# Optimization experiments

Measured on AMD Instinct MI355X. Metric: run time of the kernel, lower is better.

Reference implementation:

```python
import jax, jax.numpy as jnp
import numpy as np


def setup_inputs() -> dict:
    key = jax.random.key(0)
    k1, k2, k3 = jax.random.split(key, 3)
    B, N, F, O = 2048, 50000, 256, 24
    x = jax.random.normal(k1, (B, F), dtype=jnp.float32)
    X_train = jax.random.normal(k2, (N, F), dtype=jnp.float32)
    Y_train = jax.random.normal(k3, (N, O), dtype=jnp.float32)
    return {"x": x, "X_train": X_train, "Y_train": Y_train}


def reference(x, X_train, Y_train):
    # x: [B, F] (already flat), X_train: [N, F], Y_train: [N, O]
    B = x.shape[0]
    x_flat = x.reshape(B, -1)
    # Squared Euclidean distances via expansion: ||a||^2 + ||b||^2 - 2 a.b
    # (monotone in true distance, so argmin is identical to cdist+argmin)
    x2 = jnp.sum(x_flat * x_flat, axis=1, keepdims=True)          # [B, 1]
    t2 = jnp.sum(X_train * X_train, axis=1)                        # [N]
    cross = x_flat @ X_train.T                                     # [B, N]
    d2 = x2 + t2[None, :] - 2.0 * cross                            # [B, N]
    nearest = jnp.argmin(d2, axis=1)                               # [B]
    y_pred = Y_train[nearest]                                      # [B, O]
    return y_pred
```

## Files before the change

kernel.cpp:

```cpp
#include <hip/hip_runtime.h>
#include <stdint.h>

typedef unsigned short u16;
typedef unsigned int   u32;
typedef unsigned long long u64;

#define F_DIM 256
#define O_DIM 24
#define MARGIN  3.0f
#define FMARGIN 3.0f
#define WCAP 512
#define NWAVE_CAP 4096

#define AS1 __attribute__((address_space(1)))
#define AS3 __attribute__((address_space(3)))

typedef __bf16 bf16x8 __attribute__((ext_vector_type(8)));
typedef float  f32x4  __attribute__((ext_vector_type(4)));

__device__ __forceinline__ u32 ordf(float s) {
    u32 b = __float_as_uint(s);
    return (b & 0x80000000u) ? ~b : (b | 0x80000000u);
}
__device__ __forceinline__ float iordf(u32 e) {
    return __uint_as_float((e & 0x80000000u) ? (e ^ 0x80000000u) : ~e);
}
__device__ __forceinline__ u16 f2bf(float f) {
    u32 u = __float_as_uint(f);
    u32 r = (u + 0x7FFFu + ((u >> 16) & 1u)) >> 16;
    return (u16)r;
}

__global__ void init_kernel(u64* best, u32* gminu, int B) {
    int i = blockIdx.x * blockDim.x + threadIdx.x;
    if (i < B) { best[i] = ~0ull; if (gminu) gminu[i] = ordf(1e30f); }
}

__global__ void t2_kernel(const float* __restrict__ X, float* __restrict__ t2,
                          int N, int Npad) {
    int tid = threadIdx.x;
    int row = blockIdx.x * 4 + (tid >> 6);
    int lane = tid & 63;
    if (row >= Npad) return;
    if (row >= N) { if (lane == 0) t2[row] = 1e30f; return; }
    float4 v = ((const float4*)(X + (size_t)row * F_DIM))[lane];
    float s = v.x * v.x + v.y * v.y + v.z * v.z + v.w * v.w;
    #pragma unroll
    for (int off = 32; off > 0; off >>= 1) s += __shfl_down(s, off, 64);
    if (lane == 0) t2[row] = s;
}

__global__ __launch_bounds__(256) void convert_tile(const float* __restrict__ src,
        u16* __restrict__ dst, float* __restrict__ t2out, int nrows, int do_t2,
        u64* best, u32* gminu, int ninit) {
    __shared__ u16 tl[8192];
    const int tid = threadIdx.x;
    const int t = blockIdx.x, p = blockIdx.y;
    if (best) {
        int id = (p * gridDim.x + t) * 256 + tid;
        if (id < ninit) { best[id] = ~0ull; gminu[id] = ordf(1e30f); }
    }
    const int w = tid >> 6, L = tid & 63;
    const int col = L * 4;
    const int ks = col >> 5, j = col & 7, lhi = ((col >> 3) & 3) << 4;
    #pragma unroll
    for (int i = 0; i < 8; ++i) {
        int rloc = i * 4 + w;
        int grow = t * 128 + p * 32 + rloc;
        float4 v = make_float4(0.f, 0.f, 0.f, 0.f);
        if (grow < nrows) v = *(const float4*)(src + (size_t)grow * F_DIM + col);
        if (do_t2) {
            float s = v.x * v.x + v.y * v.y + v.z * v.z + v.w * v.w;
            #pragma unroll
            for (int off = 32; off > 0; off >>= 1) s += __shfl_down(s, off, 64);
            if (L == 0) t2out[grow] = (grow < nrows) ? s : 1e30f;
        }
        u16* q = &tl[ks * 1024 + (rloc >> 4) * 512 + (((rloc & 15) | lhi)) * 8 + j];
        q[0] = f2bf(v.x); q[1] = f2bf(v.y); q[2] = f2bf(v.z); q[3] = f2bf(v.w);
    }
    __syncthreads();
    const uint4* s4 = (const uint4*)tl;
    uint4* d4 = (uint4*)(dst + (size_t)t * 32768);
    #pragma unroll
    for (int v = 0; v < 4; ++v) {
        int lin = v * 256 + tid;
        int ksc = lin >> 7, subl = (lin >> 6) & 1, lane = lin & 63;
        d4[(ksc * 8 + 2 * p + subl) * 64 + lane] = s4[lin];
    }
}

__global__ __launch_bounds__(512, 2) void knn_mfma(
    const u16* __restrict__ xbf, const u16* __restrict__ xtbf,
    const float* __restrict__ t2, u32* __restrict__ gminu,
    u32* __restrict__ wavecnt, u64* __restrict__ cands,
    int ntiles , int nch)
{
    __shared__ u16 sB[2][8192];

    const int tid = threadIdx.x;
    const int L = tid & 63, w = tid >> 6;
    const int lid = blockIdx.x;
    const int mbcnt = (int)(gridDim.x) / nch;
    int mb, chunk;
    if (nch == 64 && mbcnt == 8) {
        const int xg = lid & 7, slot = lid >> 3;
        chunk = xg * 8 + (slot >> 3);
        mb = slot & 7;
    } else {
        mb = lid % mbcnt;
        chunk = lid / mbcnt;
    }
    const int gwave = (mb * 64 + chunk) * 8 + w;
    const int t0 = (int)(((long long)chunk * ntiles) / nch);
    const int t1 = (int)(((long long)(chunk + 1) * ntiles) / nch);

    #define TBASE_U32(nt) ((const AS1 u32*)xtbf + (size_t)((nt) >> 2) * 16384 \
                           + (size_t)(((nt) >> 1) & 1) * 1024 + (size_t)((nt) & 1) * 512)

    #define STAGE(buf, nt) do {                                                        \
        const AS1 u32* gp_ = TBASE_U32(nt);                                            \
        AS3 u32* lb_ = (AS3 u32*)&sB[buf][0];                                          \
        _Pragma("unroll")                                                              \
        for (int j = 0; j < 2; ++j) {                                                  \
            const int unit = j * 8 + w;                                                \
            __builtin_amdgcn_global_load_lds(                                          \
                gp_ + (size_t)(unit >> 1) * 2048 + (size_t)(unit & 1) * 256            \
                    + (size_t)L * 4,                                                   \
                lb_ + unit * 256, 16, 0, 0);                                           \
        }                                                                              \
    } while (0)

    STAGE(0, t0);

    bf16x8 areg[16];
    {
        const int t128 = mb * 2 + (w >> 2);
        const u16* base = xbf + (size_t)t128 * 32768 + (size_t)(w & 3) * 1024 + (size_t)L * 8;
        #pragma unroll
        for (int ks = 0; ks < 8; ++ks)
            #pragma unroll
            for (int i = 0; i < 2; ++i)
                areg[ks * 2 + i] = *(const bf16x8*)(base + ks * 4096 + i * 512);
    }

    float rowmin_reg[2][4];
    #pragma unroll
    for (int i = 0; i < 2; ++i)
        #pragma unroll
        for (int r = 0; r < 4; ++r) rowmin_reg[i][r] = 1e30f;

    u32 wcount = 0;
    u64* const wreg = cands + (size_t)gwave * WCAP;

    __syncthreads();

    for (int nt = t0; nt < t1; ++nt) {
        const int cur = (nt - t0) & 1;
        if (nt + 1 < t1) STAGE(cur ^ 1, nt + 1);

        float t2v[2];
        #pragma unroll
        for (int c = 0; c < 2; ++c) t2v[c] = t2[nt * 32 + (L & 15) + c * 16];

        f32x4 acc[2][2];
        #pragma unroll
        for (int i = 0; i < 2; ++i)
            #pragma unroll
            for (int c = 0; c < 2; ++c)
                #pragma unroll
                for (int r = 0; r < 4; ++r) acc[i][c][r] = 0.f;

        #pragma unroll
        for (int ks = 0; ks < 8; ++ks) {
            bf16x8 bc[2];
            #pragma unroll
            for (int c = 0; c < 2; ++c)
                bc[c] = *(const bf16x8*)&sB[cur][ks * 1024 + c * 512 + L * 8];
            #pragma unroll
            for (int i = 0; i < 2; ++i)
                #pragma unroll
                for (int c = 0; c < 2; ++c)
                    acc[i][c] = __builtin_amdgcn_mfma_f32_16x16x32_bf16(areg[ks * 2 + i], bc[c], acc[i][c], 0, 0, 0);
        }

        const int colb = nt * 32 + (L & 15);
        float r4[2][4];
        #pragma unroll
        for (int i = 0; i < 2; ++i) {
            #pragma unroll
            for (int r = 0; r < 4; ++r) r4[i][r] = 1e30f;
            #pragma unroll
            for (int c = 0; c < 2; ++c)
                #pragma unroll
                for (int r = 0; r < 4; ++r)
                    r4[i][r] = fminf(r4[i][r], fmaf(-2.f, acc[i][c][r], t2v[c]));
        }

        float thb[2][4];
        if (nt == t0) {
            #pragma unroll
            for (int i = 0; i < 2; ++i)
                #pragma unroll
                for (int r = 0; r < 4; ++r) rowmin_reg[i][r] = r4[i][r];
            #pragma unroll
            for (int st = 1; st <= 8; st <<= 1)
                #pragma unroll
                for (int i = 0; i < 2; ++i)
                    #pragma unroll
                    for (int r = 0; r < 4; ++r)
                        rowmin_reg[i][r] = fminf(rowmin_reg[i][r], __shfl_xor(rowmin_reg[i][r], st, 64));
            #pragma unroll
            for (int i = 0; i < 2; ++i)
                #pragma unroll
                for (int r = 0; r < 4; ++r) thb[i][r] = rowmin_reg[i][r];
        } else {
            #pragma unroll
            for (int i = 0; i < 2; ++i)
                #pragma unroll
                for (int r = 0; r < 4; ++r) thb[i][r] = fminf(rowmin_reg[i][r], r4[i][r]);
        }

        bool anyhit = false;
        #pragma unroll
        for (int i = 0; i < 2; ++i)
            #pragma unroll
            for (int r = 0; r < 4; ++r)
                anyhit = anyhit || (r4[i][r] < thb[i][r] + MARGIN);

        if (__any(anyhit)) {
            u32 cnt = 0;
            #pragma unroll
            for (int i = 0; i < 2; ++i)
                #pragma unroll
                for (int r = 0; r < 4; ++r) {
                    float th = thb[i][r] + MARGIN;
                    if (r4[i][r] < th) {
                        #pragma unroll
                        for (int c = 0; c < 2; ++c)
                            cnt += (fmaf(-2.f, acc[i][c][r], t2v[c]) < th) ? 1u : 0u;
                    }
                }
            u32 pre = cnt;
            #pragma unroll
            for (int d = 1; d < 64; d <<= 1) {
                u32 v = __shfl_up(pre, d, 64);
                if (L >= d) pre += v;
            }
            u32 total = __shfl(pre, 63, 64);
            u32 woff = wcount + pre - cnt;
            #pragma unroll
            for (int i = 0; i < 2; ++i)
                #pragma unroll
                for (int r = 0; r < 4; ++r) {
                    float th = thb[i][r] + MARGIN;
                    if (r4[i][r] < th) {
                        const int q = mb * 256 + w * 32 + i * 16 + (L >> 4) * 4 + r;
                        #pragma unroll
                        for (int c = 0; c < 2; ++c) {
                            float s = fmaf(-2.f, acc[i][c][r], t2v[c]);
                            if (s < th) {
                                if (woff < WCAP)
                                    wreg[woff] = ((u64)__float_as_uint(s) << 32)
                                               | (u64)(((u32)q << 16) | (u32)(colb + c * 16));
                                woff++;
                            }
                        }
                    }
                }
            wcount += total;
        }

        #pragma unroll
        for (int i = 0; i < 2; ++i)
            #pragma unroll
            for (int r = 0; r < 4; ++r)
                rowmin_reg[i][r] = fminf(rowmin_reg[i][r], r4[i][r]);
        if (((nt - t0) & 3) == 3) {
            #pragma unroll
            for (int st = 1; st <= 8; st <<= 1)
                #pragma unroll
                for (int i = 0; i < 2; ++i)
                    #pragma unroll
                    for (int r = 0; r < 4; ++r)
                        rowmin_reg[i][r] = fminf(rowmin_reg[i][r], __shfl_xor(rowmin_reg[i][r], st, 64));
        }

        __syncthreads();
    }

    #pragma unroll
    for (int st = 1; st <= 8; st <<= 1)
        #pragma unroll
        for (int i = 0; i < 2; ++i)
            #pragma unroll
            for (int r = 0; r < 4; ++r)
                rowmin_reg[i][r] = fminf(rowmin_reg[i][r], __shfl_xor(rowmin_reg[i][r], st, 64));
    if ((L & 15) == 0) {
        #pragma unroll
        for (int i = 0; i < 2; ++i)
            #pragma unroll
            for (int r = 0; r < 4; ++r) {
                int q = mb * 256 + w * 32 + i * 16 + (L >> 4) * 4 + r;
                atomicMin(&gminu[q], ordf(rowmin_reg[i][r]));
            }
    }
    if (L == 0) wavecnt[gwave] = (wcount < WCAP) ? wcount : WCAP;
    #undef STAGE
    #undef TBASE_U32
}

__global__ void rescore(const float* __restrict__ x, const float* __restrict__ Xt,
                        const float* __restrict__ t2, const u32* __restrict__ gminu,
                        const u32* __restrict__ wavecnt, const u64* __restrict__ cands,
                        u64* __restrict__ best) {
    const int L = threadIdx.x & 63;
    const int gw = blockIdx.x * (blockDim.x >> 6) + (threadIdx.x >> 6);
    if (gw >= NWAVE_CAP) return;
    u32 cnt = wavecnt[gw];
    if (cnt > WCAP) cnt = WCAP;
    const u64* reg = cands + (size_t)gw * WCAP;
    for (u32 base = 0; base < cnt; base += 64) {
        u32 i = base + L;
        u64 rec = 0; bool pass = false;
        if (i < cnt) {
            rec = reg[i];
            float sb = __uint_as_float((u32)(rec >> 32));
            int q = (int)((rec >> 16) & 0xFFFFu);
            pass = sb < iordf(gminu[q]) + FMARGIN;
        }
        u64 bal = __ballot(pass);
        while (bal) {
            int j = __ffsll((unsigned long long)bal) - 1;
            bal &= bal - 1;
            u64 r2 = __shfl(rec, j, 64);
            int q = (int)((r2 >> 16) & 0xFFFFu);
            int n = (int)(r2 & 0xFFFFu);
            float4 a = *((const float4*)(x  + (size_t)q * F_DIM) + L);
            float4 b = *((const float4*)(Xt + (size_t)n * F_DIM) + L);
            float d = fmaf(a.x, b.x, fmaf(a.y, b.y, fmaf(a.z, b.z, a.w * b.w)));
            #pragma unroll
            for (int st = 32; st > 0; st >>= 1) d += __shfl_xor(d, st, 64);
            if (L == 0) {
                float s = fmaf(-2.f, d, t2[n]);
                u64 p = ((u64)ordf(s) << 32) | (u32)n;
                atomicMin(&best[q], p);
            }
        }
    }
}

__global__ void gather_kernel(const float* __restrict__ Y, const u64* __restrict__ best,
                              float* __restrict__ out, int B, int N) {
    int gid = blockIdx.x * blockDim.x + threadIdx.x;
    int total = B * O_DIM;
    if (gid >= total) return;
    int b = gid / O_DIM;
    int o = gid - b * O_DIM;
    u32 n = (u32)(best[b] & 0xFFFFFFFFull);
    if (n >= (u32)N) n = 0;
    out[gid] = Y[(size_t)n * O_DIM + o];
}

#define BM 128
#define BN 128
#define BK 16
#define NSPLIT 64
#define LDA (BM + 4)

__global__ __launch_bounds__(256) void knn_main_fp32(
    const float* __restrict__ Xq, const float* __restrict__ Xt,
    const float* __restrict__ t2, u64* __restrict__ best, int N)
{
    __shared__ float As[BK][LDA];
    __shared__ float Bs[BK][LDA];
    __shared__ u64 red[BM][17];

    const int tid = threadIdx.x;
    const int tx = tid & 15;
    const int ty = tid >> 4;
    const int m0 = blockIdx.y * BM;
    const int CHUNK = (N + NSPLIT - 1) / NSPLIT;
    const int n0c = blockIdx.x * CHUNK;
    const int n1c = min(N, n0c + CHUNK);

    u64 bestv[8];
    #pragma unroll
    for (int i = 0; i < 8; ++i) bestv[i] = ~0ull;

    const int srow = tid >> 2;
    const int scol4 = (tid & 3) * 4;

    for (int nt = n0c; nt < n1c; nt += BN) {
        float accl[8][8];
        #pragma unroll
        for (int i = 0; i < 8; ++i)
            #pragma unroll
            for (int j = 0; j < 8; ++j) accl[i][j] = 0.f;
        for (int k0 = 0; k0 < F_DIM; k0 += BK) {
            #pragma unroll
            for (int h = 0; h < 2; ++h) {
                int row = h * 64 + srow;
                float4 av = *(const float4*)(Xq + (size_t)(m0 + row) * F_DIM + k0 + scol4);
                As[scol4 + 0][row] = av.x; As[scol4 + 1][row] = av.y;
                As[scol4 + 2][row] = av.z; As[scol4 + 3][row] = av.w;
                int n = nt + row;
                float4 bv = make_float4(0.f, 0.f, 0.f, 0.f);
                if (n < n1c) bv = *(const float4*)(Xt + (size_t)n * F_DIM + k0 + scol4);
                Bs[scol4 + 0][row] = bv.x; Bs[scol4 + 1][row] = bv.y;
                Bs[scol4 + 2][row] = bv.z; Bs[scol4 + 3][row] = bv.w;
            }
            __syncthreads();
            #pragma unroll
            for (int k = 0; k < BK; ++k) {
                float4 a0 = *(const float4*)&As[k][ty * 4];
                float4 a1 = *(const float4*)&As[k][64 + ty * 4];
                float4 b0 = *(const float4*)&Bs[k][tx * 4];
                float4 b1 = *(const float4*)&Bs[k][64 + tx * 4];
                float am[8] = {a0.x, a0.y, a0.z, a0.w, a1.x, a1.y, a1.z, a1.w};
                float bn[8] = {b0.x, b0.y, b0.z, b0.w, b1.x, b1.y, b1.z, b1.w};
                #pragma unroll
                for (int i = 0; i < 8; ++i)
                    #pragma unroll
                    for (int j = 0; j < 8; ++j)
                        accl[i][j] = fmaf(am[i], bn[j], accl[i][j]);
            }
            __syncthreads();
        }
        #pragma unroll
        for (int j = 0; j < 8; ++j) {
            int nl = (j < 4) ? (tx * 4 + j) : (64 + tx * 4 + (j - 4));
            int n = nt + nl;
            if (n < n1c) {
                float t2v = t2[n];
                #pragma unroll
                for (int i = 0; i < 8; ++i) {
                    float score = fmaf(-2.f, accl[i][j], t2v);
                    u64 p = ((u64)ordf(score) << 32) | (u32)n;
                    bestv[i] = (p < bestv[i]) ? p : bestv[i];
                }
            }
        }
    }
    #pragma unroll
    for (int i = 0; i < 8; ++i) {
        int ml = (i < 4) ? (ty * 4 + i) : (64 + ty * 4 + (i - 4));
        red[ml][tx] = bestv[i];
    }
    __syncthreads();
    if (tid < BM) {
        u64 b = red[tid][0];
        #pragma unroll
        for (int t = 1; t < 16; ++t) { u64 v = red[tid][t]; b = (v < b) ? v : b; }
        atomicMin(&best[m0 + tid], b);
    }
}

extern "C" void kernel_launch(void* const* d_in, const int* in_sizes, int n_in,
                              void* d_out, int out_size, void* d_ws, size_t ws_size,
                              hipStream_t stream) {
    const float* x  = (const float*)d_in[0];
    const float* Xt = (const float*)d_in[1];
    const float* Yt = (const float*)d_in[2];
    float* out = (float*)d_out;

    const int B = in_sizes[0] / F_DIM;
    const int N = in_sizes[1] / F_DIM;
    const int NT128 = (N + 127) / 128;
    const int Npad = NT128 * 128;
    const int NT64 = NT128 * 2;
    const int NT32 = NT64 * 2;
    const int MB = B / 256;
    const int MT128 = B / 128;
    const int NCH = 64;

    char* wsp = (char*)d_ws;
    size_t off = 0;
    auto nxt = [&](size_t bytes) {
        char* p = wsp + off;
        off = (off + bytes + 255) & ~(size_t)255;
        return p;
    };
    float* t2       = (float*)nxt((size_t)Npad * 4);
    u64*   best     = (u64*)  nxt((size_t)B * 8);
    u32*   wavecnt  = (u32*)  nxt((size_t)NWAVE_CAP * 4);
    u32*   gminu    = (u32*)  nxt((size_t)B * 4);
    u64*   cands    = (u64*)  nxt((size_t)NWAVE_CAP * WCAP * 8);
    u16*   xbf      = (u16*)  nxt((size_t)B * F_DIM * 2);
    u16*   xtbf     = (u16*)  nxt((size_t)Npad * F_DIM * 2);
    size_t required = off;

    if (ws_size >= required && B % 256 == 0 && MB * NCH * 8 <= NWAVE_CAP) {
        convert_tile<<<dim3(MT128, 4), 256, 0, stream>>>(x, xbf, (float*)nullptr, B, 0,
                                                         best, gminu, B);
        convert_tile<<<dim3(NT128, 4), 256, 0, stream>>>(Xt, xtbf, t2, N, 1,
                                                         (u64*)nullptr, (u32*)nullptr, 0);
        knn_mfma<<<dim3(MB * NCH), 512, 0, stream>>>(xbf, xtbf, t2, gminu, wavecnt, cands, NT32, NCH);
        rescore<<<NWAVE_CAP / 4, 256, 0, stream>>>(x, Xt, t2, gminu, wavecnt, cands, best);
    } else {
        init_kernel<<<(B + 255) / 256, 256, 0, stream>>>(best, (u32*)nullptr, B);
        t2_kernel<<<(N + 3) / 4, 256, 0, stream>>>(Xt, t2, N, N);
        dim3 grid(NSPLIT, B / BM);
        knn_main_fp32<<<grid, 256, 0, stream>>>(x, Xt, t2, best, N);
    }

    int total = B * O_DIM;
    gather_kernel<<<(total + 255) / 256, 256, 0, stream>>>(Yt, best, out, B, N);
}
```

Before: 234.3 us.

## Process two tiles per barrier with four LDS buffers and merge conversion kernels

The main MFMA loop now handles two 32-column tiles per iteration, using four LDS buffers so that two tiles are prefetched while the current pair is computed. This halves the number of __syncthreads barriers and makes the prefetch deeper. The two bf16 conversion launches are also merged into a single kernel that picks x or X_train by block index, saving one launch. The trade-off is LDS usage doubling to 64KB per block, which may cut occupancy below the two blocks per CU requested in the launch bounds.

```diff
diff --git a/kernel.cpp b/kernel.cpp
--- a/kernel.cpp
+++ b/kernel.cpp
@@ -50,15 +50,21 @@
     if (lane == 0) t2[row] = s;
 }
 
-__global__ __launch_bounds__(256) void convert_tile(const float* __restrict__ src,
-        u16* __restrict__ dst, float* __restrict__ t2out, int nrows, int do_t2,
-        u64* best, u32* gminu, int ninit) {
+__global__ __launch_bounds__(256) void convert_dual(
+        const float* __restrict__ x, u16* __restrict__ xbf, int B,
+        const float* __restrict__ Xt, u16* __restrict__ xtbf, float* __restrict__ t2out, int N,
+        int mt128, u64* best, u32* gminu) {
     __shared__ u16 tl[8192];
     const int tid = threadIdx.x;
-    const int t = blockIdx.x, p = blockIdx.y;
-    if (best) {
-        int id = (p * gridDim.x + t) * 256 + tid;
-        if (id < ninit) { best[id] = ~0ull; gminu[id] = ordf(1e30f); }
+    const int tg = blockIdx.x, p = blockIdx.y;
+    const bool isX = tg < mt128;
+    const int t = isX ? tg : tg - mt128;
+    const float* src = isX ? x : Xt;
+    u16* dst = isX ? xbf : xtbf;
+    const int nrows = isX ? B : N;
+    if (isX) {
+        int id = (p * mt128 + t) * 256 + tid;
+        if (id < B) { best[id] = ~0ull; gminu[id] = ordf(1e30f); }
     }
     const int w = tid >> 6, L = tid & 63;
     const int col = L * 4;
@@ -69,7 +75,7 @@
         int grow = t * 128 + p * 32 + rloc;
         float4 v = make_float4(0.f, 0.f, 0.f, 0.f);
         if (grow < nrows) v = *(const float4*)(src + (size_t)grow * F_DIM + col);
-        if (do_t2) {
+        if (!isX) {
             float s = v.x * v.x + v.y * v.y + v.z * v.z + v.w * v.w;
             #pragma unroll
             for (int off = 32; off > 0; off >>= 1) s += __shfl_down(s, off, 64);
@@ -95,7 +101,7 @@
     u32* __restrict__ wavecnt, u64* __restrict__ cands,
     int ntiles , int nch)
 {
-    __shared__ u16 sB[2][8192];
+    __shared__ u16 sB[4][8192];
 
     const int tid = threadIdx.x;
     const int L = tid & 63, w = tid >> 6;
@@ -131,6 +137,7 @@
     } while (0)
 
     STAGE(0, t0);
+    if (t0 + 1 < t1) STAGE(1, t0 + 1);
 
     bf16x8 areg[16];
     {
@@ -154,14 +161,7 @@
 
     __syncthreads();
 
-    for (int nt = t0; nt < t1; ++nt) {
-        const int cur = (nt - t0) & 1;
-        if (nt + 1 < t1) STAGE(cur ^ 1, nt + 1);
-
-        float t2v[2];
-        #pragma unroll
-        for (int c = 0; c < 2; ++c) t2v[c] = t2[nt * 32 + (L & 15) + c * 16];
-
+    auto process = [&](int nt, int buf, const float* t2v) {
         f32x4 acc[2][2];
         #pragma unroll
         for (int i = 0; i < 2; ++i)
@@ -175,7 +175,7 @@
             bf16x8 bc[2];
             #pragma unroll
             for (int c = 0; c < 2; ++c)
-                bc[c] = *(const bf16x8*)&sB[cur][ks * 1024 + c * 512 + L * 8];
+                bc[c] = *(const bf16x8*)&sB[buf][ks * 1024 + c * 512 + L * 8];
             #pragma unroll
             for (int i = 0; i < 2; ++i)
                 #pragma unroll
@@ -284,6 +284,24 @@
                     for (int r = 0; r < 4; ++r)
                         rowmin_reg[i][r] = fminf(rowmin_reg[i][r], __shfl_xor(rowmin_reg[i][r], st, 64));
         }
+    };
+
+    for (int nt = t0; nt < t1; nt += 2) {
+        const int cb = ((((nt - t0) >> 1) & 1) << 1);
+        const bool has2 = (nt + 1 < t1);
+
+        float t2a[2], t2b[2];
+        #pragma unroll
+        for (int c = 0; c < 2; ++c) t2a[c] = t2[nt * 32 + (L & 15) + c * 16];
+        if (has2)
+            #pragma unroll
+            for (int c = 0; c < 2; ++c) t2b[c] = t2[(nt + 1) * 32 + (L & 15) + c * 16];
+
+        if (nt + 2 < t1) STAGE(cb ^ 2, nt + 2);
+        if (nt + 3 < t1) STAGE((cb ^ 2) + 1, nt + 3);
+
+        process(nt, cb, t2a);
+        if (has2) process(nt + 1, cb + 1, t2b);
 
         __syncthreads();
     }
@@ -490,10 +508,8 @@
     size_t required = off;
 
     if (ws_size >= required && B % 256 == 0 && MB * NCH * 8 <= NWAVE_CAP) {
-        convert_tile<<<dim3(MT128, 4), 256, 0, stream>>>(x, xbf, (float*)nullptr, B, 0,
-                                                         best, gminu, B);
-        convert_tile<<<dim3(NT128, 4), 256, 0, stream>>>(Xt, xtbf, t2, N, 1,
-                                                         (u64*)nullptr, (u32*)nullptr, 0);
+        convert_dual<<<dim3(MT128 + NT128, 4), 256, 0, stream>>>(
+            x, xbf, B, Xt, xtbf, t2, N, MT128, best, gminu);
         knn_mfma<<<dim3(MB * NCH), 512, 0, stream>>>(xbf, xtbf, t2, gminu, wavecnt, cands, NT32, NCH);
         rescore<<<NWAVE_CAP / 4, 256, 0, stream>>>(x, Xt, t2, gminu, wavecnt, cands, best);
     } else {
```

After: 214.9 us. -8.3%, faster.
